# Performance work log

Hardware: AMD Instinct MI355X
Metric: run time of the kernel (lower is better)

The kernel has to match this reference:

```python
import jax, jax.numpy as jnp
import numpy as np

B, S, D, H, L, K = 16, 384, 512, 8, 4, 7
HD = D // H
MAXLEN = 400


def _pos_encoding(d=D, max_len=MAXLEN):
    # Faithful to the (unusual) torch loop: even idx i -> sin(pos/10000**(2i/d)),
    # odd idx i+1 -> cos(pos/10000**(2(i+1)/d))
    pe = np.zeros((max_len, d), dtype=np.float32)
    pos = np.arange(max_len, dtype=np.float64)[:, None]
    i = np.arange(0, d, 2)
    pe[:, i] = np.sin(pos / 10000.0 ** (2 * i / d))
    pe[:, i + 1] = np.cos(pos / 10000.0 ** (2 * (i + 1) / d))
    return jnp.asarray(pe)

POS_ENC = _pos_encoding()


def layer_norm(x, g, b, eps=1e-5):
    m = jnp.mean(x, -1, keepdims=True)
    v = jnp.mean((x - m) ** 2, -1, keepdims=True)
    return (x - m) * jax.lax.rsqrt(v + eps) * g + b


def dsconv(x, dw_w, pw_w, pw_b):
    # x: [B,S,D]; depthwise conv1d (no bias) then pointwise 1x1 (bias)
    xc = jnp.transpose(x, (0, 2, 1))  # [B,D,S]
    y = jax.lax.conv_general_dilated(
        xc, dw_w, window_strides=(1,), padding=[(K // 2, K // 2)],
        dimension_numbers=("NCH", "OIH", "NCH"), feature_group_count=D)  # [B,D,S]
    return jnp.einsum("bcs,oc->bso", y, pw_w) + pw_b  # [B,S,D]


def setup_inputs():
    key = jax.random.key(0)
    ks = jax.random.split(key, 16)
    sc = 0.02
    inp = {
        "x": jax.random.normal(ks[0], (B, S, D), jnp.float32),
        "mask": jax.random.randint(ks[1], (B, S), 0, 2, jnp.int32),
        "dw_w": jax.random.normal(ks[2], (L, D, 1, K), jnp.float32) * sc,
        "pw_w": jax.random.normal(ks[3], (L, D, D), jnp.float32) * sc,
        "pw_b": jnp.zeros((L, D), jnp.float32),
        "conv_ln_g": jnp.ones((L, D), jnp.float32),
        "conv_ln_b": jnp.zeros((L, D), jnp.float32),
        "pos_ln_g": jnp.ones((D,), jnp.float32),
        "pos_ln_b": jnp.zeros((D,), jnp.float32),
        "wq": jax.random.normal(ks[4], (D, D), jnp.float32) * sc,
        "bq": jnp.zeros((D,), jnp.float32),
        "wk": jax.random.normal(ks[5], (D, D), jnp.float32) * sc,
        "bk": jnp.zeros((D,), jnp.float32),
        "wv": jax.random.normal(ks[6], (D, D), jnp.float32) * sc,
        "bv": jnp.zeros((D,), jnp.float32),
        "wo": jax.random.normal(ks[7], (D, D), jnp.float32) * sc,
        "bo": jnp.zeros((D,), jnp.float32),
        "ff_ln_g": jnp.ones((D,), jnp.float32),
        "ff_ln_b": jnp.zeros((D,), jnp.float32),
        "ff_w": jax.random.normal(ks[8], (D, D), jnp.float32) * sc,
        "ff_b": jnp.zeros((D,), jnp.float32),
    }
    return inp


def attention(x, mask, wq, bq, wk, bk, wv, bv, wo, bo):
    def heads(w, b):
        y = jnp.einsum("bsd,od->bso", x, w) + b
        return jnp.transpose(y.reshape(B, S, H, HD), (0, 2, 1, 3))  # [B,H,S,HD]
    q, k, v = heads(wq, bq), heads(wk, bk), heads(wv, bv)
    energy = jnp.einsum("bhqd,bhkd->bhqk", q, k) / jnp.sqrt(jnp.float32(HD))
    m = (mask == 1)[:, None, None, :]  # [B,1,1,S]
    energy = jnp.where(m, jnp.float32(-1e10), energy)
    alpha = jax.nn.softmax(energy, axis=-1)  # dropout = identity (eval)
    a = jnp.einsum("bhqk,bhkd->bhqd", alpha, v)
    a = jnp.transpose(a, (0, 2, 1, 3)).reshape(B, S, D)
    return jnp.einsum("bsd,od->bso", a, wo) + bo


def reference(x, mask, dw_w, pw_w, pw_b, conv_ln_g, conv_ln_b, pos_ln_g, pos_ln_b,
              wq, bq, wk, bk, wv, bv, wo, bo, ff_ln_g, ff_ln_b, ff_w, ff_b):
    out = x + POS_ENC[None, :S, :]
    res = out
    out = layer_norm(out, pos_ln_g, pos_ln_b)
    for i in range(L):
        out = jax.nn.relu(dsconv(out, dw_w[i], pw_w[i], pw_b[i]))
        out = out + res  # dropout = identity (eval)
        res = out
        out = layer_norm(out, conv_ln_g[i], conv_ln_b[i])
    out = attention(out, mask, wq, bq, wk, bk, wv, bv, wo, bo)
    out = out + res
    res = out
    out = layer_norm(out, ff_ln_g, ff_ln_b)
    out = jax.nn.relu(jnp.einsum("bsd,od->bso", out, ff_w) + ff_b)
    return out + res
```

## Files before the change

kernel.cpp:

```cpp
#include <hip/hip_runtime.h>

#define BB 16
#define SS 384
#define DD 512
#define HH 8
#define HDIM 64
#define LLAY 4
#define KW 7
#define MM (BB*SS)

typedef unsigned short u16;
typedef unsigned int u32;
typedef short short8v __attribute__((ext_vector_type(8)));
typedef float floatx4 __attribute__((ext_vector_type(4)));

__device__ __forceinline__ float bf2f(u16 u) {
    union { u32 i; float f; } v; v.i = ((u32)u) << 16; return v.f;
}
__device__ __forceinline__ u16 f2bf(float f) {
    union { float f; u32 i; } v; v.f = f;
    return (u16)((v.i + 0x7FFFu + ((v.i >> 16) & 1u)) >> 16);
}
__device__ __forceinline__ bool sniff_f32(const void* dtp) {
    return *((const u32*)dtp) == 0x3F800000u;
}
__device__ __forceinline__ float ldf(const void* p, long i, bool f32) {
    return f32 ? ((const float*)p)[i] : bf2f(((const u16*)p)[i]);
}
__device__ __forceinline__ short8v ldfrag_scalar(const void* p, long i, bool f32) {
    short8v r;
    if (f32) {
        const float* q = (const float*)p + i;
#pragma unroll
        for (int j = 0; j < 8; j++) r[j] = (short)f2bf(q[j]);
    } else {
        r = *(const short8v*)((const u16*)p + i);
    }
    return r;
}

__device__ __forceinline__ void load_lds16(const u16* g, u16* l) {
    __builtin_amdgcn_global_load_lds((const __attribute__((address_space(1))) void*)g,
                                     (__attribute__((address_space(3))) void*)l, 16, 0, 0);
}
__device__ __forceinline__ int swz(int row) { return (row & 3) ^ ((row >> 2) & 3); }
__device__ __forceinline__ short8v lds_frag(const u16* buf, int row, int quad) {
    return *(const short8v*)(buf + ((size_t)row * 4 + (quad ^ swz(row))) * 8);
}

__device__ __forceinline__ floatx4 mfma16(short8v a, short8v b, floatx4 c) {
    return __builtin_amdgcn_mfma_f32_16x16x32_bf16(a, b, c, 0, 0, 0);
}

#define WCV_DW 2359296
#define WCV_TOT (WCV_DW + LLAY*KW*DD)
#define NCVB ((WCV_TOT + 255) / 256)
#define NUVB 512
#define NZB  96
#define NSTATS (4 * MM)

__global__ __launch_bounds__(256) void posln_cvt_kernel(
    const void* __restrict__ x, const void* __restrict__ g, const void* __restrict__ bvec,
    u16* __restrict__ res, u16* __restrict__ out,
    const void* __restrict__ pw_w, const void* __restrict__ wq,
    const void* __restrict__ wk, const void* __restrict__ wv,
    const void* __restrict__ wo, const void* __restrict__ ff_w,
    const void* __restrict__ dw_w, u16* __restrict__ wdst,
    float* __restrict__ uvp, float* __restrict__ statsp,
    const void* __restrict__ cln_g, const void* __restrict__ cln_b,
    const void* __restrict__ fln_g, const void* __restrict__ fln_b,
    const void* __restrict__ dtp) {
    const bool f32 = sniff_f32(dtp);
    const int tid = threadIdx.x;
    if (blockIdx.x >= MM) {
        const int ib = blockIdx.x - MM;
        if (ib < NCVB) {
            const int i = ib * 256 + tid;
            if (i >= WCV_TOT) return;
            const void* src; long idx; float scale = 1.f;
            if (i < 1048576) { src = pw_w; idx = i; }
            else if (i < WCV_DW) {
                const int j = i - 1048576;
                const int m = j >> 18;
                idx = j & 262143;
                src = (m == 0) ? wq : (m == 1) ? wk : (m == 2) ? wv : (m == 3) ? wo : ff_w;
                const int k = (int)(idx & 511);
                if (m <= 2)      scale = ldf(cln_g, 1536 + k, f32);
                else if (m == 4) scale = ldf(fln_g, k, f32);
            } else {
                const int j = i - WCV_DW;
                const int l = j / (KW * DD);
                const int r1 = j % (KW * DD);
                const int t = r1 / DD, c = r1 % DD;
                src = dw_w; idx = ((long)l * DD + c) * KW + t;
            }
            wdst[i] = f2bf(scale * ldf(src, idx, f32));
        } else if (ib < NCVB + NUVB) {
            const int i2 = ib - NCVB;
            const int wave = tid >> 6, lane = tid & 63;
            const int gn = i2 * 4 + wave;
            const int mat = gn >> 9, n = gn & 511;
            const void* srcm = (mat == 0) ? wq : (mat == 1) ? wk : (mat == 2) ? wv : ff_w;
            float su = 0.f, sv = 0.f;
#pragma unroll
            for (int e = 0; e < 8; e++) {
                const int k = lane * 8 + e;
                const float w = ldf(srcm, (long)n * 512 + k, f32);
                const float gg = (mat < 3) ? ldf(cln_g, 1536 + k, f32) : ldf(fln_g, k, f32);
                const float bb = (mat < 3) ? ldf(cln_b, 1536 + k, f32) : ldf(fln_b, k, f32);
                su += gg * w; sv += bb * w;
            }
#pragma unroll
            for (int off = 32; off; off >>= 1) { su += __shfl_xor(su, off); sv += __shfl_xor(sv, off); }
            if (lane == 0) { uvp[mat * 1024 + n] = su; uvp[mat * 1024 + 512 + n] = sv; }
        } else {
            const int idx = (ib - NCVB - NUVB) * 256 + tid;
            if (idx < NSTATS) statsp[idx] = 0.f;
        }
        return;
    }
    const int row = blockIdx.x;
    const int s = row % SS;
    float v[2];
#pragma unroll
    for (int i = 0; i < 2; i++) {
        const int d = tid + i * 256;
        const float freq = __expf(-(float)d * 0.035977892078032f);
        const float arg = (float)s * freq;
        const float pe = (d & 1) ? __cosf(arg) : __sinf(arg);
        v[i] = ldf(x, (long)row * DD + d, f32) + pe;
        res[row * DD + d] = f2bf(v[i]);
    }
    if (out == nullptr) return;
    float sum = v[0] + v[1], sq = v[0] * v[0] + v[1] * v[1];
#pragma unroll
    for (int off = 32; off; off >>= 1) { sum += __shfl_down(sum, off); sq += __shfl_down(sq, off); }
    __shared__ float red[4][2];
    const int wv2 = tid >> 6;
    if ((tid & 63) == 0) { red[wv2][0] = sum; red[wv2][1] = sq; }
    __syncthreads();
    sum = red[0][0] + red[1][0] + red[2][0] + red[3][0];
    sq  = red[0][1] + red[1][1] + red[2][1] + red[3][1];
    const float mean = sum * (1.f / DD);
    const float rstd = rsqrtf(sq * (1.f / DD) - mean * mean + 1e-5f);
#pragma unroll
    for (int i = 0; i < 2; i++) {
        const int d = tid + i * 256;
        out[row * DD + d] = f2bf((v[i] - mean) * rstd * ldf(g, d, f32) + ldf(bvec, d, f32));
    }
}

__global__ __launch_bounds__(256) void dwln_kernel(
    const u16* __restrict__ res, const u16* __restrict__ wdw ,
    const void* __restrict__ g, const void* __restrict__ bvec, int voff,
    u16* __restrict__ out, const void* __restrict__ dtp) {
    const bool f32 = sniff_f32(dtp);
    __shared__ __align__(16) u16 rows[14][DD];
    const int tid = threadIdx.x;
    const int lane = tid & 63, wave = tid >> 6;
    const int m0 = blockIdx.x * 8;
#pragma unroll
    for (int j = 0; j < 4; j++) {
        const int c = j * 256 + tid;
        if (c < 896) {
            int gr = m0 - 3 + (c >> 6);
            gr = (gr < 0) ? 0 : (gr >= MM ? MM - 1 : gr);
            load_lds16(res + (size_t)gr * DD + (c & 63) * 8, &rows[0][0] + (size_t)c * 8);
        }
    }
    float gv[8], bv[8];
#pragma unroll
    for (int e = 0; e < 8; e++) {
        gv[e] = ldf(g, (long)voff + lane * 8 + e, f32);
        bv[e] = ldf(bvec, (long)voff + lane * 8 + e, f32);
    }
    asm volatile("s_waitcnt vmcnt(0)\n\ts_barrier" ::: "memory");
    for (int j = wave; j < 14; j += 4) {
        const short8v v = *(const short8v*)&rows[j][lane * 8];
        float f[8], s = 0.f, q = 0.f;
#pragma unroll
        for (int e = 0; e < 8; e++) { f[e] = bf2f((u16)v[e]); s += f[e]; q += f[e] * f[e]; }
#pragma unroll
        for (int off = 32; off; off >>= 1) { s += __shfl_xor(s, off); q += __shfl_xor(q, off); }
        const float mean = s * (1.f / DD);
        const float rstd = rsqrtf(q * (1.f / DD) - mean * mean + 1e-5f);
        short8v o;
#pragma unroll
        for (int e = 0; e < 8; e++) o[e] = (short)f2bf((f[e] - mean) * rstd * gv[e] + bv[e]);
        *(short8v*)&rows[j][lane * 8] = o;
    }
    asm volatile("s_waitcnt lgkmcnt(0)\n\ts_barrier" ::: "memory");
    short8v wv[KW];
#pragma unroll
    for (int t = 0; t < KW; t++) wv[t] = *(const short8v*)(wdw + t * DD + lane * 8);
#pragma unroll
    for (int rr = wave; rr < 8; rr += 4) {
        const int gm = m0 + rr, s = gm % SS;
        float acc[8] = {0, 0, 0, 0, 0, 0, 0, 0};
#pragma unroll
        for (int t = 0; t < KW; t++) {
            const int ss2 = s + t - 3;
            if (ss2 >= 0 && ss2 < SS) {
                const short8v iv = *(const short8v*)&rows[rr + t][lane * 8];
#pragma unroll
                for (int e = 0; e < 8; e++) acc[e] += bf2f((u16)iv[e]) * bf2f((u16)wv[t][e]);
            }
        }
        short8v ov;
#pragma unroll
        for (int e = 0; e < 8; e++) ov[e] = (short)f2bf(acc[e]);
        *(short8v*)(out + (size_t)gm * DD + lane * 8) = ov;
    }
}

__global__ __launch_bounds__(256) void dwconv_kernel(const u16* __restrict__ in,
                                                     const void* __restrict__ w, int layer,
                                                     u16* __restrict__ out,
                                                     const void* __restrict__ dtp) {
    const bool f32 = sniff_f32(dtp);
    const long woff = (long)layer * DD * KW;
    const int idx = blockIdx.x * 256 + threadIdx.x;
    const int c = idx & (DD - 1);
    const int ms = idx >> 9;
    const int s = ms % SS;
    float acc = 0.f;
#pragma unroll
    for (int t = 0; t < KW; t++) {
        const int ss2 = s + t - 3;
        if (ss2 >= 0 && ss2 < SS)
            acc += bf2f(in[(ms + t - 3) * DD + c]) * ldf(w, woff + c * KW + t, f32);
    }
    out[idx] = f2bf(acc);
}

#define ASTG (64 * 32)
#define WSTG (128 * 32)
__device__ __forceinline__ void stage64(const u16* A, const u16* Wp, int m0,
                                        u16* Ab, u16* Wb, int tid, int k0) {
#pragma unroll
    for (int j = 0; j < 2; j++) {
        const int c = j * 256 + tid;
        const int row = c >> 2;
        const int kp = (c & 3) ^ swz(row);
        load_lds16(Wp + (size_t)row * DD + k0 + kp * 8, Wb + (size_t)c * 8);
    }
    {
        const int row = tid >> 2;
        const int kp = (tid & 3) ^ swz(row);
        load_lds16(A + (size_t)(m0 + row) * DD + k0 + kp * 8, Ab + (size_t)tid * 8);
    }
}

__device__ __forceinline__ void kloop64(const u16* A, const u16* Wp, int m0,
                                        u16* Abuf, u16* Wbuf,
                                        int tid, int wm, int wn, int ln15, int quad,
                                        floatx4 acc[2][4]) {
    stage64(A, Wp, m0, Abuf, Wbuf, tid, 0);
    stage64(A, Wp, m0, Abuf + ASTG, Wbuf + WSTG, tid, 32);
    stage64(A, Wp, m0, Abuf + 2 * ASTG, Wbuf + 2 * WSTG, tid, 64);
#pragma unroll
    for (int ks = 0; ks < 16; ks++) {
        const int cur = ks & 3;
        u16* Ab = Abuf + cur * ASTG;
        u16* Wb = Wbuf + cur * WSTG;
        if (ks < 13) {
            const int nxt = (ks + 3) & 3;
            stage64(A, Wp, m0, Abuf + nxt * ASTG, Wbuf + nxt * WSTG, tid, (ks + 3) * 32);
            asm volatile("s_waitcnt vmcnt(9)\n\ts_barrier" ::: "memory");
        } else if (ks == 13) {
            asm volatile("s_waitcnt vmcnt(6)\n\ts_barrier" ::: "memory");
        } else if (ks == 14) {
            asm volatile("s_waitcnt vmcnt(3)\n\ts_barrier" ::: "memory");
        } else {
            asm volatile("s_waitcnt vmcnt(0)\n\ts_barrier" ::: "memory");
        }
        const short8v a0 = lds_frag(Ab, wm * 32 + ln15, quad);
        const short8v a1 = lds_frag(Ab, wm * 32 + 16 + ln15, quad);
#pragma unroll
        for (int nt = 0; nt < 4; nt++) {
            const short8v b = lds_frag(Wb, wn * 64 + nt * 16 + ln15, quad);
            acc[0][nt] = mfma16(a0, b, acc[0][nt]);
            acc[1][nt] = mfma16(a1, b, acc[1][nt]);
        }
        asm volatile("s_waitcnt lgkmcnt(0)\n\ts_barrier" ::: "memory");
    }
}

template <int RELU, int FINAL, int STATS, int LNF>
__global__ __launch_bounds__(256, 2) void gemm64_kernel(
    const u16* __restrict__ A, const u16* __restrict__ W,
    const void* __restrict__ bias, int blayer,
    const u16* __restrict__ res_in, u16* __restrict__ res_out,
    void* __restrict__ out,
    const float* __restrict__ uvf,
    const float* __restrict__ sin_sum, const float* __restrict__ sin_sq,
    float* __restrict__ so_sum, float* __restrict__ so_sq,
    const void* __restrict__ dtp) {
    const bool f32 = sniff_f32(dtp);
    const long voff = (long)blayer * DD;
    __shared__ __align__(16) u16 smem[4 * (ASTG + WSTG)];
    u16* Wbuf = smem;
    u16* Abuf = smem + 4 * WSTG;
    const int tid = threadIdx.x;
    const int m0 = blockIdx.x * 64, n0 = blockIdx.y * 128;
    const int wave = tid >> 6, lane = tid & 63;
    const int wm = wave >> 1, wn = wave & 1;
    const int ln15 = lane & 15, quad = lane >> 4;

    floatx4 acc[2][4];
#pragma unroll
    for (int mt = 0; mt < 2; mt++)
#pragma unroll
        for (int nt = 0; nt < 4; nt++) acc[mt][nt] = {0.f, 0.f, 0.f, 0.f};

    kloop64(A, W + (size_t)n0 * DD, m0, Abuf, Wbuf, tid, wm, wn, ln15, quad, acc);

    float mu[2][4], rs[2][4];
    if constexpr (LNF) {
#pragma unroll
        for (int mt = 0; mt < 2; mt++)
#pragma unroll
            for (int r = 0; r < 4; r++) {
                const int m = m0 + wm * 32 + mt * 16 + quad * 4 + r;
                const float s = sin_sum[m] * (1.f / DD);
                const float q = sin_sq[m] * (1.f / DD);
                mu[mt][r] = s;
                rs[mt][r] = rsqrtf(q - s * s + 1e-5f);
            }
    }
    float st[2][4], sq2[2][4];
    if constexpr (STATS) {
#pragma unroll
        for (int mt = 0; mt < 2; mt++)
#pragma unroll
            for (int r = 0; r < 4; r++) { st[mt][r] = 0.f; sq2[mt][r] = 0.f; }
    }
#pragma unroll
    for (int nt = 0; nt < 4; nt++) {
        const int col = n0 + wn * 64 + nt * 16 + ln15;
        const float bval = ldf(bias, voff + col, f32);
#pragma unroll
        for (int mt = 0; mt < 2; mt++)
#pragma unroll
            for (int r = 0; r < 4; r++) {
                const int m = m0 + wm * 32 + mt * 16 + quad * 4 + r;
                float y = acc[mt][nt][r];
                if constexpr (LNF)
                    y = rs[mt][r] * y - rs[mt][r] * mu[mt][r] * uvf[col] + uvf[512 + col] + bval;
                else
                    y += bval;
                if (RELU) y = fmaxf(y, 0.f);
                y += bf2f(res_in[(size_t)m * DD + col]);
                if (res_out) res_out[(size_t)m * DD + col] = f2bf(y);
                if constexpr (FINAL) {
                    if (f32) ((float*)out)[(size_t)m * DD + col] = y;
                    else     ((u16*)out)[(size_t)m * DD + col] = f2bf(y);
                }
                if constexpr (STATS) { st[mt][r] += y; sq2[mt][r] += y * y; }
            }
    }
    if constexpr (STATS) {
#pragma unroll
        for (int mt = 0; mt < 2; mt++)
#pragma unroll
            for (int r = 0; r < 4; r++) {
                float s = st[mt][r], q = sq2[mt][r];
#pragma unroll
                for (int off = 1; off < 16; off <<= 1) {
                    s += __shfl_xor(s, off, 16);
                    q += __shfl_xor(q, off, 16);
                }
                if (ln15 == 0) {
                    const int m = m0 + wm * 32 + mt * 16 + quad * 4 + r;
                    atomicAdd(&so_sum[m], s);
                    atomicAdd(&so_sq[m], q);
                }
            }
    }
}

#define VP 72
__global__ __launch_bounds__(256, 2) void qkv64_kernel(
    const u16* __restrict__ A,
    const u16* __restrict__ Wq, const u16* __restrict__ Wk, const u16* __restrict__ Wv,
    const void* __restrict__ bq, const void* __restrict__ bk, const void* __restrict__ bv,
    u16* __restrict__ qo, u16* __restrict__ ko, u16* __restrict__ vo,
    const float* __restrict__ uvp,
    const float* __restrict__ ssum, const float* __restrict__ ssq,
    const void* __restrict__ dtp) {
    const bool f32 = sniff_f32(dtp);
    const int sel = blockIdx.z;
    const u16* W = (sel == 0) ? Wq : (sel == 1) ? Wk : Wv;
    const void* bias = (sel == 0) ? bq : (sel == 1) ? bk : bv;
    const float* uvf = uvp + sel * 1024;

    __shared__ __align__(16) u16 smem[4 * (ASTG + WSTG)];
    u16* Wbuf = smem;
    u16* Abuf = smem + 4 * WSTG;
    u16 (*vtile)[VP] = (u16 (*)[VP])smem;

    const int tid = threadIdx.x;
    const int m0 = blockIdx.x * 64, n0 = blockIdx.y * 128;
    const int wave = tid >> 6, lane = tid & 63;
    const int wm = wave >> 1, wn = wave & 1;
    const int ln15 = lane & 15, quad = lane >> 4;
    const int bidx = m0 / SS;

    floatx4 acc[2][4];
#pragma unroll
    for (int mt = 0; mt < 2; mt++)
#pragma unroll
        for (int nt = 0; nt < 4; nt++) acc[mt][nt] = {0.f, 0.f, 0.f, 0.f};

    kloop64(A, W + (size_t)n0 * DD, m0, Abuf, Wbuf, tid, wm, wn, ln15, quad, acc);

    float mu[2][4], rs[2][4];
#pragma unroll
    for (int mt = 0; mt < 2; mt++)
#pragma unroll
        for (int r = 0; r < 4; r++) {
            const int m = m0 + wm * 32 + mt * 16 + quad * 4 + r;
            const float s = ssum[m] * (1.f / DD);
            const float q = ssq[m] * (1.f / DD);
            mu[mt][r] = s;
            rs[mt][r] = rsqrtf(q - s * s + 1e-5f);
        }

    if (sel == 2) {
#pragma unroll
        for (int nt = 0; nt < 4; nt++) {
            const int cl = wn * 64 + nt * 16 + ln15;
            const int col = n0 + cl;
            const float bval = ldf(bias, col, f32);
#pragma unroll
            for (int mt = 0; mt < 2; mt++)
#pragma unroll
                for (int r = 0; r < 4; r++) {
                    const float y = rs[mt][r] * acc[mt][nt][r]
                                  - rs[mt][r] * mu[mt][r] * uvf[col] + uvf[512 + col] + bval;
                    vtile[cl][wm * 32 + mt * 16 + quad * 4 + r] = f2bf(y);
                }
        }
        __syncthreads();
        const int c = tid & 127, half = tid >> 7;
        const int col = n0 + c;
        const int h = col >> 6, hd = col & 63;
        u16* dst = vo + ((size_t)(bidx * HH + h) * HDIM + hd) * SS
                      + (m0 - bidx * SS) + half * 32;
        const u16* srcl = &vtile[c][half * 32];
#pragma unroll
        for (int j = 0; j < 4; j++)
            *(short8v*)(dst + j * 8) = *(const short8v*)(srcl + j * 8);
    } else {
        u16* out = (sel == 0) ? qo : ko;
#pragma unroll
        for (int nt = 0; nt < 4; nt++) {
            const int col = n0 + wn * 64 + nt * 16 + ln15;
            const int h = col >> 6, hd = col & 63;
            const float bval = ldf(bias, col, f32);
#pragma unroll
            for (int mt = 0; mt < 2; mt++)
#pragma unroll
                for (int r = 0; r < 4; r++) {
                    const int m = m0 + wm * 32 + mt * 16 + quad * 4 + r;
                    const int s = m - bidx * SS;
                    const float y = rs[mt][r] * acc[mt][nt][r]
                                  - rs[mt][r] * mu[mt][r] * uvf[col] + uvf[512 + col] + bval;
                    out[((size_t)(bidx * HH + h) * SS + s) * HDIM + hd] = f2bf(y);
                }
        }
    }
}

template <int RELU, int DO_LN, int FINAL>
__global__ __launch_bounds__(512, 4) void gemm16_kernel(
    const u16* __restrict__ A, const void* __restrict__ W, int wlayer,
    const void* __restrict__ bias, const void* __restrict__ g,
    const void* __restrict__ bvec, int blayer,
    const u16* __restrict__ res_in, u16* __restrict__ res_out,
    void* __restrict__ out, const void* __restrict__ dtp) {
    const bool f32 = sniff_f32(dtp);
    const long woff = (long)wlayer * DD * DD;
    const long voff = (long)blayer * DD;
    __shared__ float part[8][16][2];
    const int tid = threadIdx.x;
    const int m0 = blockIdx.x * 16;
    const int wave = tid >> 6, lane = tid & 63;
    const int ln15 = lane & 15, quad = lane >> 4;

    floatx4 acc[4];
#pragma unroll
    for (int nt = 0; nt < 4; nt++) acc[nt] = {0.f, 0.f, 0.f, 0.f};

    const u16* A0 = A + (size_t)(m0 + ln15) * DD + quad * 8;
#pragma unroll
    for (int ks = 0; ks < 16; ks++) {
        const int k0 = ks * 32;
        short8v a0 = *(const short8v*)(A0 + k0);
        short8v b[4];
#pragma unroll
        for (int nt = 0; nt < 4; nt++) {
            const long wrow = woff + (long)(wave * 64 + nt * 16 + ln15) * DD + quad * 8 + k0;
            b[nt] = ldfrag_scalar(W, wrow, f32);
        }
#pragma unroll
        for (int nt = 0; nt < 4; nt++)
            acc[nt] = mfma16(a0, b[nt], acc[nt]);
    }

#pragma unroll
    for (int nt = 0; nt < 4; nt++) {
        const int col = wave * 64 + nt * 16 + ln15;
        const float bval = ldf(bias, voff + col, f32);
#pragma unroll
        for (int r = 0; r < 4; r++) {
            const int m = m0 + quad * 4 + r;
            float y = acc[nt][r] + bval;
            if (RELU) y = fmaxf(y, 0.f);
            y += bf2f(res_in[(size_t)m * DD + col]);
            if (res_out) res_out[(size_t)m * DD + col] = f2bf(y);
            acc[nt][r] = y;
        }
    }
    if constexpr (DO_LN) {
        float ls[4], lq[4];
#pragma unroll
        for (int r = 0; r < 4; r++) {
            float s = 0.f, q = 0.f;
#pragma unroll
            for (int nt = 0; nt < 4; nt++) { const float y = acc[nt][r]; s += y; q += y * y; }
            ls[r] = s; lq[r] = q;
        }
#pragma unroll
        for (int off = 1; off < 16; off <<= 1)
#pragma unroll
            for (int r = 0; r < 4; r++) {
                ls[r] += __shfl_xor(ls[r], off);
                lq[r] += __shfl_xor(lq[r], off);
            }
        if (ln15 == 0) {
#pragma unroll
            for (int r = 0; r < 4; r++) {
                part[wave][quad * 4 + r][0] = ls[r];
                part[wave][quad * 4 + r][1] = lq[r];
            }
        }
        __syncthreads();
        float mean[4], rstd[4];
#pragma unroll
        for (int r = 0; r < 4; r++) {
            const int rr = quad * 4 + r;
            float s = 0.f, q = 0.f;
#pragma unroll
            for (int wv = 0; wv < 8; wv++) { s += part[wv][rr][0]; q += part[wv][rr][1]; }
            const float mn = s * (1.f / DD);
            mean[r] = mn;
            rstd[r] = rsqrtf(q * (1.f / DD) - mn * mn + 1e-5f);
        }
#pragma unroll
        for (int nt = 0; nt < 4; nt++) {
            const int col = wave * 64 + nt * 16 + ln15;
            const float gv = ldf(g, voff + col, f32);
            const float bv = ldf(bvec, voff + col, f32);
#pragma unroll
            for (int r = 0; r < 4; r++) {
                const int m = m0 + quad * 4 + r;
                ((u16*)out)[(size_t)m * DD + col] =
                    f2bf((acc[nt][r] - mean[r]) * rstd[r] * gv + bv);
            }
        }
    } else {
#pragma unroll
        for (int nt = 0; nt < 4; nt++) {
            const int col = wave * 64 + nt * 16 + ln15;
#pragma unroll
            for (int r = 0; r < 4; r++) {
                const int m = m0 + quad * 4 + r;
                if (FINAL && f32) ((float*)out)[(size_t)m * DD + col] = acc[nt][r];
                else              ((u16*)out)[(size_t)m * DD + col] = f2bf(acc[nt][r]);
            }
        }
    }
}

__global__ __launch_bounds__(512, 4) void qkv16_kernel(
    const u16* __restrict__ A,
    const void* __restrict__ Wq, const void* __restrict__ Wk, const void* __restrict__ Wv,
    const void* __restrict__ bq, const void* __restrict__ bk, const void* __restrict__ bv,
    u16* __restrict__ qo, u16* __restrict__ ko, u16* __restrict__ vo,
    const void* __restrict__ dtp) {
    const bool f32 = sniff_f32(dtp);
    const int sel = blockIdx.y;
    const void* W = (sel == 0) ? Wq : (sel == 1) ? Wk : Wv;
    const void* bias = (sel == 0) ? bq : (sel == 1) ? bk : bv;

    const int tid = threadIdx.x;
    const int m0 = blockIdx.x * 16;
    const int wave = tid >> 6, lane = tid & 63;
    const int ln15 = lane & 15, quad = lane >> 4;
    const int bidx = m0 / SS;

    floatx4 acc[4];
#pragma unroll
    for (int nt = 0; nt < 4; nt++) acc[nt] = {0.f, 0.f, 0.f, 0.f};

    const u16* A0 = A + (size_t)(m0 + ln15) * DD + quad * 8;
#pragma unroll
    for (int ks = 0; ks < 16; ks++) {
        const int k0 = ks * 32;
        short8v a0 = *(const short8v*)(A0 + k0);
        short8v b[4];
#pragma unroll
        for (int nt = 0; nt < 4; nt++) {
            const long wrow = (long)(wave * 64 + nt * 16 + ln15) * DD + quad * 8 + k0;
            b[nt] = ldfrag_scalar(W, wrow, f32);
        }
#pragma unroll
        for (int nt = 0; nt < 4; nt++)
            acc[nt] = mfma16(a0, b[nt], acc[nt]);
    }

    if (sel == 2) {
#pragma unroll
        for (int nt = 0; nt < 4; nt++) {
            const int col = wave * 64 + nt * 16 + ln15;
            const int h = col >> 6, hd = col & 63;
            const float bval = ldf(bias, col, f32);
#pragma unroll
            for (int r = 0; r < 4; r++) {
                const int m = m0 + quad * 4 + r;
                const int s = m - bidx * SS;
                vo[((size_t)(bidx * HH + h) * HDIM + hd) * SS + s] = f2bf(acc[nt][r] + bval);
            }
        }
    } else {
        u16* out = (sel == 0) ? qo : ko;
#pragma unroll
        for (int nt = 0; nt < 4; nt++) {
            const int col = wave * 64 + nt * 16 + ln15;
            const int h = col >> 6, hd = col & 63;
            const float bval = ldf(bias, col, f32);
#pragma unroll
            for (int r = 0; r < 4; r++) {
                const int m = m0 + quad * 4 + r;
                const int s = m - bidx * SS;
                out[((size_t)(bidx * HH + h) * SS + s) * HDIM + hd] = f2bf(acc[nt][r] + bval);
            }
        }
    }
}

#define ALP 392
__global__ __launch_bounds__(256) void attn_kernel(const u16* __restrict__ q,
                                                   const u16* __restrict__ k,
                                                   const u16* __restrict__ vT,
                                                   const int* __restrict__ mask,
                                                   u16* __restrict__ out) {
    __shared__ __align__(16) u16 Kb[3072 * 8];
    __shared__ __align__(16) u16 Vb[3072 * 8];
    __shared__ __align__(16) u16 al4[4][16][ALP];

    const int n = blockIdx.x;
    const int i = n >> 3;
    const int g = (n & 7) * 16 + i / 6;
    const int sub = i % 6;
    const int h = g & 7, b = g >> 3;
    const int tid = threadIdx.x;
    const int wave = tid >> 6, lane = tid & 63;
    const int ln15 = lane & 15, quad = lane >> 4;
    const int q0 = (sub * 4 + wave) * 16;

    const u16* qh = q + (size_t)(b * HH + h) * SS * HDIM;
    const u16* kh = k + (size_t)(b * HH + h) * SS * HDIM;
    const u16* vh = vT + (size_t)(b * HH + h) * HDIM * SS;

#pragma unroll
    for (int j = 0; j < 12; j++) {
        const int c = j * 256 + tid;
        const int row = c >> 3, cc = c & 7;
        const int kp = cc ^ ((row ^ (row >> 3)) & 7);
        load_lds16(kh + (size_t)row * HDIM + kp * 8, Kb + (size_t)c * 8);
    }
#pragma unroll
    for (int j = 0; j < 12; j++) {
        const int c = j * 256 + tid;
        const int tile = c >> 8, rr = (c >> 2) & 63, cc = c & 3;
        const int kp = cc ^ swz(rr);
        load_lds16(vh + (size_t)rr * SS + tile * 32 + kp * 8, Vb + (size_t)c * 8);
    }
    const short8v* arow = (const short8v*)(qh + (q0 + ln15) * HDIM + quad * 8);
    const short8v a0 = arow[0], a1 = arow[4];
    __syncthreads();

    floatx4 sc[24];
#pragma unroll
    for (int t = 0; t < 24; t++) {
        const int row = t * 16 + ln15;
        const int s3 = (row ^ (row >> 3)) & 7;
        const short8v b0 = *(const short8v*)(Kb + ((size_t)row * 8 + (quad ^ s3)) * 8);
        const short8v b1 = *(const short8v*)(Kb + ((size_t)row * 8 + ((4 + quad) ^ s3)) * 8);
        floatx4 acc = {0.f, 0.f, 0.f, 0.f};
        acc = mfma16(a0, b0, acc);
        acc = mfma16(a1, b1, acc);
        sc[t] = acc;
    }
    float mx[4] = {-3.0e38f, -3.0e38f, -3.0e38f, -3.0e38f};
#pragma unroll
    for (int t = 0; t < 24; t++) {
        const bool msk = (mask[b * SS + t * 16 + ln15] == 1);
#pragma unroll
        for (int r = 0; r < 4; r++) {
            float v = sc[t][r] * 0.125f;
            if (msk) v = -1e10f;
            sc[t][r] = v;
            mx[r] = fmaxf(mx[r], v);
        }
    }
#pragma unroll
    for (int off = 8; off; off >>= 1)
#pragma unroll
        for (int r = 0; r < 4; r++) mx[r] = fmaxf(mx[r], __shfl_xor(mx[r], off, 16));
    float sum[4] = {0.f, 0.f, 0.f, 0.f};
    u16* alw = &al4[wave][0][0];
#pragma unroll
    for (int t = 0; t < 24; t++) {
#pragma unroll
        for (int r = 0; r < 4; r++) {
            const float p = __expf(sc[t][r] - mx[r]);
            sum[r] += p;
            alw[(quad * 4 + r) * ALP + t * 16 + ln15] = f2bf(p);
        }
    }
#pragma unroll
    for (int off = 8; off; off >>= 1)
#pragma unroll
        for (int r = 0; r < 4; r++) sum[r] += __shfl_xor(sum[r], off, 16);
    __builtin_amdgcn_s_waitcnt(0);

#pragma unroll
    for (int dt = 0; dt < 4; dt++) {
        floatx4 acc = {0.f, 0.f, 0.f, 0.f};
        const int row = dt * 16 + ln15;
        const int vsw = quad ^ swz(row);
#pragma unroll
        for (int c2 = 0; c2 < 12; c2++) {
            const short8v af = *(const short8v*)(alw + ln15 * ALP + c2 * 32 + quad * 8);
            const short8v bf = *(const short8v*)(Vb + ((size_t)c2 * 256 + row * 4 + vsw) * 8);
            acc = mfma16(af, bf, acc);
        }
#pragma unroll
        for (int rr = 0; rr < 4; rr++) {
            const int s = q0 + quad * 4 + rr;
            out[((size_t)(b * SS + s)) * DD + h * HDIM + dt * 16 + ln15] = f2bf(acc[rr] / sum[rr]);
        }
    }
}

extern "C" void kernel_launch(void* const* d_in, const int* in_sizes, int n_in,
                              void* d_out, int out_size, void* d_ws, size_t ws_size,
                              hipStream_t stream) {
    (void)in_sizes; (void)n_in; (void)out_size;
    const void* x     = d_in[0];
    const int*  mask  = (const int*)d_in[1];
    const void* dw_w  = d_in[2];
    const void* pw_w  = d_in[3];
    const void* pw_b  = d_in[4];
    const void* cln_g = d_in[5];
    const void* cln_b = d_in[6];
    const void* pln_g = d_in[7];
    const void* pln_b = d_in[8];
    const void* wq    = d_in[9];
    const void* bq    = d_in[10];
    const void* wk    = d_in[11];
    const void* bk    = d_in[12];
    const void* wv    = d_in[13];
    const void* bv    = d_in[14];
    const void* wo    = d_in[15];
    const void* bo    = d_in[16];
    const void* fln_g = d_in[17];
    const void* fln_b = d_in[18];
    const void* ff_w  = d_in[19];
    const void* ff_b  = d_in[20];
    const void* dtp   = cln_g;

    const size_t nAct = (size_t)MM * DD;
    char* p = (char*)d_ws;
    u16* res   = (u16*)p; p += nAct * 2;
    u16* lnout = (u16*)p; p += nAct * 2;
    u16* tmp   = (u16*)p; p += nAct * 2;
    u16* vT    = (u16*)p; p += nAct * 2;
    u16* wcv   = (u16*)p; p += (size_t)WCV_TOT * 2;
    float* uvp    = (float*)p; p += 4096 * 4;
    float* statsp = (float*)p;
    float* sA_sum = statsp;
    float* sA_sq  = statsp + MM;
    float* sB_sum = statsp + 2 * MM;
    float* sB_sq  = statsp + 3 * MM;
    u16* kb    = (u16*)d_out;

    const size_t needFast = nAct * 2 * 4 + (size_t)WCV_TOT * 2 + (4096 + NSTATS) * 4;
    const bool fast = (ws_size >= needFast);

    if (fast) {
        posln_cvt_kernel<<<MM + NCVB + NUVB + NZB, 256, 0, stream>>>(
            x, pln_g, pln_b, res, nullptr ,
            pw_w, wq, wk, wv, wo, ff_w, dw_w, wcv, uvp, statsp,
            cln_g, cln_b, fln_g, fln_b, dtp);
        const u16* w_pw = wcv;
        const u16* w_q  = wcv + 1048576;
        const u16* w_k  = wcv + 1310720;
        const u16* w_v  = wcv + 1572864;
        const u16* w_o  = wcv + 1835008;
        const u16* w_ff = wcv + 2097152;
        const u16* w_dw = wcv + WCV_DW;

        for (int i = 0; i < LLAY - 1; i++) {
            const void* lg = (i == 0) ? pln_g : cln_g;
            const void* lb = (i == 0) ? pln_b : cln_b;
            const int lo = (i == 0) ? 0 : (i - 1) * DD;
            dwln_kernel<<<MM / 8, 256, 0, stream>>>(
                res, w_dw + (size_t)i * KW * DD, lg, lb, lo, tmp, dtp);
            gemm64_kernel<1, 0, 0, 0><<<dim3(MM / 64, 4), 256, 0, stream>>>(
                tmp, w_pw + (size_t)i * DD * DD, pw_b, i, res, res, nullptr,
                nullptr, nullptr, nullptr, nullptr, nullptr, dtp);
        }
        dwln_kernel<<<MM / 8, 256, 0, stream>>>(
            res, w_dw + (size_t)3 * KW * DD, cln_g, cln_b, 2 * DD, tmp, dtp);
        gemm64_kernel<1, 0, 1, 0><<<dim3(MM / 64, 4), 256, 0, stream>>>(
            tmp, w_pw + (size_t)3 * DD * DD, pw_b, 3, res, res, nullptr,
            nullptr, nullptr, nullptr, sA_sum, sA_sq, dtp);

        qkv64_kernel<<<dim3(MM / 64, 4, 3), 256, 0, stream>>>(
            res, w_q, w_k, w_v, bq, bk, bv, tmp, kb, vT, uvp, sA_sum, sA_sq, dtp);

        attn_kernel<<<BB * HH * (SS / 64), 256, 0, stream>>>(tmp, kb, vT, mask, lnout);

        gemm64_kernel<0, 0, 1, 0><<<dim3(MM / 64, 4), 256, 0, stream>>>(
            lnout, w_o, bo, 0, res, res, nullptr,
            nullptr, nullptr, nullptr, sB_sum, sB_sq, dtp);
        gemm64_kernel<1, 1, 0, 1><<<dim3(MM / 64, 4), 256, 0, stream>>>(
            res, w_ff, ff_b, 0, res, nullptr, d_out,
            uvp + 3 * 1024, sB_sum, sB_sq, nullptr, nullptr, dtp);
    } else {
        posln_cvt_kernel<<<MM, 256, 0, stream>>>(
            x, pln_g, pln_b, res, lnout,
            pw_w, wq, wk, wv, wo, ff_w, dw_w, (u16*)d_ws, uvp, statsp,
            cln_g, cln_b, fln_g, fln_b, dtp);
        for (int i = 0; i < LLAY; i++) {
            dwconv_kernel<<<MM * DD / 256, 256, 0, stream>>>(lnout, dw_w, i, tmp, dtp);
            gemm16_kernel<1, 1, 0><<<MM / 16, 512, 0, stream>>>(
                tmp, pw_w, i, pw_b, cln_g, cln_b, i, res, res, lnout, dtp);
        }
        qkv16_kernel<<<dim3(MM / 16, 3), 512, 0, stream>>>(
            lnout, wq, wk, wv, bq, bk, bv, tmp, kb, vT, dtp);

        attn_kernel<<<BB * HH * (SS / 64), 256, 0, stream>>>(tmp, kb, vT, mask, lnout);

        gemm16_kernel<0, 1, 0><<<MM / 16, 512, 0, stream>>>(
            lnout, wo, 0, bo, fln_g, fln_b, 0, res, res, lnout, dtp);
        gemm16_kernel<1, 0, 1><<<MM / 16, 512, 0, stream>>>(
            lnout, ff_w, 0, ff_b, nullptr, nullptr, 0, res, nullptr, d_out, dtp);
    }
}
```

Baseline: 309.5 us.

## Fuse positional encoding into first dwconv, skip bf16 weight copies, remap blocks per XCD

Removes the per-row positional-encoding pass from the prep kernel and computes x+PE inside the first depthwise-conv/LN kernel, which also writes the residual. When inputs are already bf16, the pointwise and output-projection weights are read directly from the originals rather than converted copies. GEMM and QKV kernels switch to a flat 1D grid with an XCD-aware block-to-tile mapping for better L2 locality. The fused PE path uses scalar element loads rather than the async LDS loads, which may be slower for that one kernel.

```diff
diff --git a/kernel.cpp b/kernel.cpp
--- a/kernel.cpp
+++ b/kernel.cpp
@@ -58,10 +58,11 @@
 #define NUVB 512
 #define NZB  96
 #define NSTATS (4 * MM)
+#define NAUX (NCVB + NUVB + NZB)
 
 __global__ __launch_bounds__(256) void posln_cvt_kernel(
     const void* __restrict__ x, const void* __restrict__ g, const void* __restrict__ bvec,
-    u16* __restrict__ res, u16* __restrict__ out,
+    u16* __restrict__ res, u16* __restrict__ out, int npos,
     const void* __restrict__ pw_w, const void* __restrict__ wq,
     const void* __restrict__ wk, const void* __restrict__ wv,
     const void* __restrict__ wo, const void* __restrict__ ff_w,
@@ -72,13 +73,13 @@
     const void* __restrict__ dtp) {
     const bool f32 = sniff_f32(dtp);
     const int tid = threadIdx.x;
-    if (blockIdx.x >= MM) {
-        const int ib = blockIdx.x - MM;
+    if (blockIdx.x >= npos) {
+        const int ib = blockIdx.x - npos;
         if (ib < NCVB) {
             const int i = ib * 256 + tid;
             if (i >= WCV_TOT) return;
-            const void* src; long idx; float scale = 1.f;
-            if (i < 1048576) { src = pw_w; idx = i; }
+            const void* src; long idx; float scale = 1.f; bool skip = false;
+            if (i < 1048576) { src = pw_w; idx = i; skip = !f32; }
             else if (i < WCV_DW) {
                 const int j = i - 1048576;
                 const int m = j >> 18;
@@ -87,6 +88,7 @@
                 const int k = (int)(idx & 511);
                 if (m <= 2)      scale = ldf(cln_g, 1536 + k, f32);
                 else if (m == 4) scale = ldf(fln_g, k, f32);
+                else             skip = !f32;
             } else {
                 const int j = i - WCV_DW;
                 const int l = j / (KW * DD);
@@ -94,7 +96,7 @@
                 const int t = r1 / DD, c = r1 % DD;
                 src = dw_w; idx = ((long)l * DD + c) * KW + t;
             }
-            wdst[i] = f2bf(scale * ldf(src, idx, f32));
+            if (!skip) wdst[i] = f2bf(scale * ldf(src, idx, f32));
         } else if (ib < NCVB + NUVB) {
             const int i2 = ib - NCVB;
             const int wave = tid >> 6, lane = tid & 63;
@@ -131,7 +133,6 @@
         v[i] = ldf(x, (long)row * DD + d, f32) + pe;
         res[row * DD + d] = f2bf(v[i]);
     }
-    if (out == nullptr) return;
     float sum = v[0] + v[1], sq = v[0] * v[0] + v[1] * v[1];
 #pragma unroll
     for (int off = 32; off; off >>= 1) { sum += __shfl_down(sum, off); sq += __shfl_down(sq, off); }
@@ -150,23 +151,47 @@
     }
 }
 
+template <int PE0>
 __global__ __launch_bounds__(256) void dwln_kernel(
-    const u16* __restrict__ res, const u16* __restrict__ wdw ,
+    const u16* __restrict__ res, const void* __restrict__ xsrc,
+    u16* __restrict__ res_out,
+    const u16* __restrict__ wdw ,
     const void* __restrict__ g, const void* __restrict__ bvec, int voff,
     u16* __restrict__ out, const void* __restrict__ dtp) {
     const bool f32 = sniff_f32(dtp);
     __shared__ __align__(16) u16 rows[14][DD];
     const int tid = threadIdx.x;
     const int lane = tid & 63, wave = tid >> 6;
-    const int m0 = blockIdx.x * 8;
-#pragma unroll
-    for (int j = 0; j < 4; j++) {
-        const int c = j * 256 + tid;
-        if (c < 896) {
-            int gr = m0 - 3 + (c >> 6);
-            gr = (gr < 0) ? 0 : (gr >= MM ? MM - 1 : gr);
-            load_lds16(res + (size_t)gr * DD + (c & 63) * 8, &rows[0][0] + (size_t)c * 8);
-        }
+    const int bsw = (blockIdx.x & 7) * 96 + (blockIdx.x >> 3);
+    const int m0 = bsw * 8;
+    if constexpr (PE0) {
+        const int d0 = tid * 2;
+        const float fr0 = __expf(-(float)d0 * 0.035977892078032f);
+        const float fr1 = __expf(-(float)(d0 + 1) * 0.035977892078032f);
+        for (int j = 0; j < 14; j++) {
+            const int gr0 = m0 - 3 + j;
+            const int gr = (gr0 < 0) ? 0 : (gr0 >= MM ? MM - 1 : gr0);
+            const int s = gr % SS;
+            const float pe0 = __sinf((float)s * fr0);
+            const float pe1 = __cosf((float)s * fr1);
+            const u16 b0 = f2bf(ldf(xsrc, (long)gr * DD + d0, f32) + pe0);
+            const u16 b1 = f2bf(ldf(xsrc, (long)gr * DD + d0 + 1, f32) + pe1);
+            rows[j][d0] = b0; rows[j][d0 + 1] = b1;
+            if (j >= 3 && j < 11)
+                *(u32*)(res_out + (size_t)gr * DD + d0) = (u32)b0 | ((u32)b1 << 16);
+        }
+        __syncthreads();
+    } else {
+#pragma unroll
+        for (int j = 0; j < 4; j++) {
+            const int c = j * 256 + tid;
+            if (c < 896) {
+                int gr = m0 - 3 + (c >> 6);
+                gr = (gr < 0) ? 0 : (gr >= MM ? MM - 1 : gr);
+                load_lds16(res + (size_t)gr * DD + (c & 63) * 8, &rows[0][0] + (size_t)c * 8);
+            }
+        }
+        asm volatile("s_waitcnt vmcnt(0)\n\ts_barrier" ::: "memory");
     }
     float gv[8], bv[8];
 #pragma unroll
@@ -174,7 +199,6 @@
         gv[e] = ldf(g, (long)voff + lane * 8 + e, f32);
         bv[e] = ldf(bvec, (long)voff + lane * 8 + e, f32);
     }
-    asm volatile("s_waitcnt vmcnt(0)\n\ts_barrier" ::: "memory");
     for (int j = wave; j < 14; j += 4) {
         const short8v v = *(const short8v*)&rows[j][lane * 8];
         float f[8], s = 0.f, q = 0.f;
@@ -289,6 +313,7 @@
 template <int RELU, int FINAL, int STATS, int LNF>
 __global__ __launch_bounds__(256, 2) void gemm64_kernel(
     const u16* __restrict__ A, const u16* __restrict__ W,
+    const void* __restrict__ Worig, int wlayer,
     const void* __restrict__ bias, int blayer,
     const u16* __restrict__ res_in, u16* __restrict__ res_out,
     void* __restrict__ out,
@@ -302,18 +327,24 @@
     u16* Wbuf = smem;
     u16* Abuf = smem + 4 * WSTG;
     const int tid = threadIdx.x;
-    const int m0 = blockIdx.x * 64, n0 = blockIdx.y * 128;
+    const int flat = blockIdx.x;
+    const int xcd = flat & 7, ii = flat >> 3;
+    const int m0 = (xcd * 12 + (ii >> 2)) * 64;
+    const int n0 = (ii & 3) * 128;
     const int wave = tid >> 6, lane = tid & 63;
     const int wm = wave >> 1, wn = wave & 1;
     const int ln15 = lane & 15, quad = lane >> 4;
 
+    const u16* Wbase = (!f32 && Worig)
+        ? ((const u16*)Worig + (size_t)wlayer * DD * DD) : W;
+
     floatx4 acc[2][4];
 #pragma unroll
     for (int mt = 0; mt < 2; mt++)
 #pragma unroll
         for (int nt = 0; nt < 4; nt++) acc[mt][nt] = {0.f, 0.f, 0.f, 0.f};
 
-    kloop64(A, W + (size_t)n0 * DD, m0, Abuf, Wbuf, tid, wm, wn, ln15, quad, acc);
+    kloop64(A, Wbase + (size_t)n0 * DD, m0, Abuf, Wbuf, tid, wm, wn, ln15, quad, acc);
 
     float mu[2][4], rs[2][4];
     if constexpr (LNF) {
@@ -389,7 +420,12 @@
     const float* __restrict__ ssum, const float* __restrict__ ssq,
     const void* __restrict__ dtp) {
     const bool f32 = sniff_f32(dtp);
-    const int sel = blockIdx.z;
+    const int flat = blockIdx.x;
+    const int xcd = flat & 7, ii = flat >> 3;
+    const int mloc = ii / 12, rem = ii % 12;
+    const int sel = rem >> 2;
+    const int n0 = (rem & 3) * 128;
+    const int m0 = (xcd * 12 + mloc) * 64;
     const u16* W = (sel == 0) ? Wq : (sel == 1) ? Wk : Wv;
     const void* bias = (sel == 0) ? bq : (sel == 1) ? bk : bv;
     const float* uvf = uvp + sel * 1024;
@@ -400,7 +436,6 @@
     u16 (*vtile)[VP] = (u16 (*)[VP])smem;
 
     const int tid = threadIdx.x;
-    const int m0 = blockIdx.x * 64, n0 = blockIdx.y * 128;
     const int wave = tid >> 6, lane = tid & 63;
     const int wm = wave >> 1, wn = wave & 1;
     const int ln15 = lane & 15, quad = lane >> 4;
@@ -802,8 +837,8 @@
     const bool fast = (ws_size >= needFast);
 
     if (fast) {
-        posln_cvt_kernel<<<MM + NCVB + NUVB + NZB, 256, 0, stream>>>(
-            x, pln_g, pln_b, res, nullptr ,
+        posln_cvt_kernel<<<NAUX, 256, 0, stream>>>(
+            x, pln_g, pln_b, res, nullptr, 0,
             pw_w, wq, wk, wv, wo, ff_w, dw_w, wcv, uvp, statsp,
             cln_g, cln_b, fln_g, fln_b, dtp);
         const u16* w_pw = wcv;
@@ -814,36 +849,40 @@
         const u16* w_ff = wcv + 2097152;
         const u16* w_dw = wcv + WCV_DW;
 
-        for (int i = 0; i < LLAY - 1; i++) {
-            const void* lg = (i == 0) ? pln_g : cln_g;
-            const void* lb = (i == 0) ? pln_b : cln_b;
-            const int lo = (i == 0) ? 0 : (i - 1) * DD;
-            dwln_kernel<<<MM / 8, 256, 0, stream>>>(
-                res, w_dw + (size_t)i * KW * DD, lg, lb, lo, tmp, dtp);
-            gemm64_kernel<1, 0, 0, 0><<<dim3(MM / 64, 4), 256, 0, stream>>>(
-                tmp, w_pw + (size_t)i * DD * DD, pw_b, i, res, res, nullptr,
+        dwln_kernel<1><<<MM / 8, 256, 0, stream>>>(
+            nullptr, x, res, w_dw, pln_g, pln_b, 0, tmp, dtp);
+        gemm64_kernel<1, 0, 0, 0><<<384, 256, 0, stream>>>(
+            tmp, w_pw, pw_w, 0, pw_b, 0, res, res, nullptr,
+            nullptr, nullptr, nullptr, nullptr, nullptr, dtp);
+        for (int i = 1; i < LLAY - 1; i++) {
+            dwln_kernel<0><<<MM / 8, 256, 0, stream>>>(
+                res, nullptr, nullptr, w_dw + (size_t)i * KW * DD,
+                cln_g, cln_b, (i - 1) * DD, tmp, dtp);
+            gemm64_kernel<1, 0, 0, 0><<<384, 256, 0, stream>>>(
+                tmp, w_pw + (size_t)i * DD * DD, pw_w, i, pw_b, i, res, res, nullptr,
                 nullptr, nullptr, nullptr, nullptr, nullptr, dtp);
         }
-        dwln_kernel<<<MM / 8, 256, 0, stream>>>(
-            res, w_dw + (size_t)3 * KW * DD, cln_g, cln_b, 2 * DD, tmp, dtp);
-        gemm64_kernel<1, 0, 1, 0><<<dim3(MM / 64, 4), 256, 0, stream>>>(
-            tmp, w_pw + (size_t)3 * DD * DD, pw_b, 3, res, res, nullptr,
+        dwln_kernel<0><<<MM / 8, 256, 0, stream>>>(
+            res, nullptr, nullptr, w_dw + (size_t)3 * KW * DD,
+            cln_g, cln_b, 2 * DD, tmp, dtp);
+        gemm64_kernel<1, 0, 1, 0><<<384, 256, 0, stream>>>(
+            tmp, w_pw + (size_t)3 * DD * DD, pw_w, 3, pw_b, 3, res, res, nullptr,
             nullptr, nullptr, nullptr, sA_sum, sA_sq, dtp);
 
-        qkv64_kernel<<<dim3(MM / 64, 4, 3), 256, 0, stream>>>(
+        qkv64_kernel<<<1152, 256, 0, stream>>>(
             res, w_q, w_k, w_v, bq, bk, bv, tmp, kb, vT, uvp, sA_sum, sA_sq, dtp);
 
         attn_kernel<<<BB * HH * (SS / 64), 256, 0, stream>>>(tmp, kb, vT, mask, lnout);
 
-        gemm64_kernel<0, 0, 1, 0><<<dim3(MM / 64, 4), 256, 0, stream>>>(
-            lnout, w_o, bo, 0, res, res, nullptr,
+        gemm64_kernel<0, 0, 1, 0><<<384, 256, 0, stream>>>(
+            lnout, w_o, wo, 0, bo, 0, res, res, nullptr,
             nullptr, nullptr, nullptr, sB_sum, sB_sq, dtp);
-        gemm64_kernel<1, 1, 0, 1><<<dim3(MM / 64, 4), 256, 0, stream>>>(
-            res, w_ff, ff_b, 0, res, nullptr, d_out,
+        gemm64_kernel<1, 1, 0, 1><<<384, 256, 0, stream>>>(
+            res, w_ff, nullptr, 0, ff_b, 0, res, nullptr, d_out,
             uvp + 3 * 1024, sB_sum, sB_sq, nullptr, nullptr, dtp);
     } else {
         posln_cvt_kernel<<<MM, 256, 0, stream>>>(
-            x, pln_g, pln_b, res, lnout,
+            x, pln_g, pln_b, res, lnout, MM,
             pw_w, wq, wk, wv, wo, ff_w, dw_w, (u16*)d_ws, uvp, statsp,
             cln_g, cln_b, fln_g, fln_b, dtp);
         for (int i = 0; i < LLAY; i++) {
```

Result: slower. 322.4 us (+4.2%).
